# Performance work log

Hardware: AMD Instinct MI355X
Metric: run time of the kernel (lower is better)

## Reference

```python
import jax, jax.numpy as jnp
import numpy as np

B, S, D = 4, 4096, 1024

def setup_inputs() -> dict:
    key = jax.random.key(0)
    k1, k2, k3 = jax.random.split(key, 3)
    x = jax.random.normal(k1, (B, S, D), dtype=jnp.float32)
    # torch nn.Linear weights: [out_features, in_features], scaled for sanity
    W_qkv = jax.random.normal(k2, (3 * D, D), dtype=jnp.float32) * (1.0 / np.sqrt(D))
    W_o = jax.random.normal(k3, (D, D), dtype=jnp.float32) * (1.0 / np.sqrt(D))
    return {"x": x, "W_qkv": W_qkv, "W_o": W_o}


def reference(x, W_qkv, W_o):
    d_model = x.shape[-1]
    # torch Linear: y = x @ W.T
    qkv = jnp.einsum("bsd,ed->bse", x, W_qkv)  # [B, S, 3D]
    Q, K, V = jnp.split(qkv, 3, axis=-1)
    scale = 1.0 / jnp.sqrt(jnp.asarray(d_model, dtype=x.dtype))
    logits = jnp.einsum("bqd,bkd->bqk", Q, K) * scale  # [B, S, S]
    weights = jax.nn.softmax(logits, axis=-1)
    attn = jnp.einsum("bqk,bkd->bqd", weights, V)  # [B, S, D]
    out = jnp.einsum("bsd,ed->bse", attn, W_o)  # [B, S, D]
    return out
```

## Files before the change

kernel.cpp:

```cpp
#include <hip/hip_runtime.h>
#include <hip/hip_bf16.h>
#include <stdint.h>

typedef unsigned short u16;
typedef __bf16 bf16x8 __attribute__((ext_vector_type(8)));
typedef unsigned short u16x8 __attribute__((ext_vector_type(8)));
typedef float f32x4 __attribute__((ext_vector_type(4)));

__device__ __forceinline__ float bf2f(u16 h) {
  union { uint32_t u; float f; } x;
  x.u = ((uint32_t)h) << 16;
  return x.f;
}
__device__ __forceinline__ u16 f2bf(float f) {
  union { float f; uint32_t u; } x;
  x.f = f;
  uint32_t r = x.u + 0x7FFFu + ((x.u >> 16) & 1u);
  return (u16)(r >> 16);
}

__device__ __forceinline__ void gload_lds16(const u16* g, u16* l) {
  __builtin_amdgcn_global_load_lds(
      (const __attribute__((address_space(1))) uint32_t*)g,
      (__attribute__((address_space(3))) uint32_t*)l, 16, 0, 0);
}

__global__ __launch_bounds__(256) void cvt_all(
    const float* __restrict__ x, const float* __restrict__ w1,
    const float* __restrict__ w2, u16* __restrict__ xb,
    u16* __restrict__ w1b, u16* __restrict__ w2b, int n1, int n2, int n3) {
  int i = blockIdx.x * 256 + threadIdx.x;
  const float* src;
  u16* dst;
  int j = i;
  if (i < n1) { src = x; dst = xb; }
  else if (i < n1 + n2) { src = w1; dst = w1b; j = i - n1; }
  else if (i < n1 + n2 + n3) { src = w2; dst = w2b; j = i - n1 - n2; }
  else return;
  const float4* p = (const float4*)src + (size_t)j * 2;
  float4 a = p[0], b = p[1];
  u16x8 o;
  o[0] = f2bf(a.x); o[1] = f2bf(a.y); o[2] = f2bf(a.z); o[3] = f2bf(a.w);
  o[4] = f2bf(b.x); o[5] = f2bf(b.y); o[6] = f2bf(b.z); o[7] = f2bf(b.w);
  ((u16x8*)dst)[j] = o;
}

template <typename OT, int EPI>
__global__ __launch_bounds__(256) void gemm_bt(
    const u16* __restrict__ A, int lda, long zsA,
    const u16* __restrict__ B, int ldb, long zsB,
    OT* __restrict__ C, int ldc, long zsC,
    int K, float scale, const float* __restrict__ rs) {
  const int z = blockIdx.z;
  A += (long)z * zsA;
  B += (long)z * zsB;
  C += (long)z * zsC;
  if constexpr (EPI == 2) rs += (long)z * 4096;

  __shared__ __align__(16) u16 As[2 * 128 * 32];
  __shared__ __align__(16) u16 Bs[2 * 128 * 32];
  const int tid  = threadIdx.x;
  const int m0   = blockIdx.y * 128;
  const int n0   = blockIdx.x * 128;
  const int wave = tid >> 6;
  const int lane = tid & 63;
  const int wm   = (wave >> 1) * 64;
  const int wn   = (wave & 1) * 64;
  const int l15  = lane & 15;
  const int quad = lane >> 4;

  f32x4 acc[4][4];
#pragma unroll
  for (int i = 0; i < 4; ++i)
#pragma unroll
    for (int j = 0; j < 4; ++j) acc[i][j] = f32x4{0.f, 0.f, 0.f, 0.f};

  const u16* gA0 = A + (size_t)(m0 + (tid >> 2)) * lda + (tid & 3) * 8;
  const u16* gA1 = A + (size_t)(m0 + 64 + (tid >> 2)) * lda + (tid & 3) * 8;
  const u16* gB0 = B + (size_t)(n0 + (tid >> 2)) * ldb + (tid & 3) * 8;
  const u16* gB1 = B + (size_t)(n0 + 64 + (tid >> 2)) * ldb + (tid & 3) * 8;
  u16* lA0 = As + tid * 8;
  u16* lA1 = As + (256 + tid) * 8;
  u16* lB0 = Bs + tid * 8;
  u16* lB1 = Bs + (256 + tid) * 8;

  for (int k0 = 0; k0 < K; k0 += 64) {
    __syncthreads();
#pragma unroll
    for (int s = 0; s < 2; ++s) {
      gload_lds16(gA0 + k0 + s * 32, lA0 + s * 4096);
      gload_lds16(gA1 + k0 + s * 32, lA1 + s * 4096);
      gload_lds16(gB0 + k0 + s * 32, lB0 + s * 4096);
      gload_lds16(gB1 + k0 + s * 32, lB1 + s * 4096);
    }
    __syncthreads();

#pragma unroll
    for (int s = 0; s < 2; ++s) {
      u16x8 a[4], b[4];
#pragma unroll
      for (int i = 0; i < 4; ++i)
        a[i] = *(const u16x8*)(As + s * 4096 + (wm + i * 16 + l15) * 32 + quad * 8);
#pragma unroll
      for (int j = 0; j < 4; ++j)
        b[j] = *(const u16x8*)(Bs + s * 4096 + (wn + j * 16 + l15) * 32 + quad * 8);
#pragma unroll
      for (int i = 0; i < 4; ++i)
#pragma unroll
        for (int j = 0; j < 4; ++j)
          acc[i][j] = __builtin_amdgcn_mfma_f32_16x16x32_bf16(
              __builtin_bit_cast(bf16x8, a[i]), __builtin_bit_cast(bf16x8, b[j]),
              acc[i][j], 0, 0, 0);
    }
  }

#pragma unroll
  for (int i = 0; i < 4; ++i) {
#pragma unroll
    for (int r = 0; r < 4; ++r) {
      const int row = m0 + wm + i * 16 + quad * 4 + r;
      float mul = scale;
      if constexpr (EPI == 2) mul = scale / rs[row];
      const size_t ro = (size_t)row * ldc;
#pragma unroll
      for (int j = 0; j < 4; ++j) {
        float v = acc[i][j][r] * mul;
        if constexpr (EPI == 1) v = __expf(v);
        const int col = n0 + wn + j * 16 + l15;
        if constexpr (__is_same(OT, float))
          C[ro + col] = v;
        else
          C[ro + col] = f2bf(v);
      }
    }
  }
}

#define BAR() __builtin_amdgcn_s_barrier()
#define PRIO(n) __builtin_amdgcn_s_setprio(n)
#define WAITV(n) asm volatile("s_waitcnt vmcnt(" #n ")" ::: "memory")

#define STG(c, h, q, t)                                                         \
  gload_lds16(((h) < 2 ? gAs : gBs) +                                           \
                  (size_t)(((h) & 1) * 128 + (q) * 64) * ((h) < 2 ? lda : ldb) + \
                  (size_t)(t) * 64,                                             \
              lds + (c) * 32768 + ((h) < 2 ? 0 : 16384) +                       \
                  (((h) & 1) * 8 + (q) * 4) * 1024 + wsub * 512)

#define LDA_Q(c, qm)                                                            \
  {                                                                             \
    _Pragma("unroll") for (int ii = 0; ii < 4; ++ii) {                          \
      _Pragma("unroll") for (int kk = 0; kk < 2; ++kk)                          \
          a[(qm) * 4 + ii][kk] = *(const u16x8*)(lds + (c) * 32768 +            \
              ((wm8 + (qm) * 4 + ii) * 2 + kk) * 512 + rq);                     \
    }                                                                           \
  }

#define LDB_Q(c, qn)                                                            \
  {                                                                             \
    _Pragma("unroll") for (int jj = 0; jj < 2; ++jj) {                          \
      _Pragma("unroll") for (int kk = 0; kk < 2; ++kk)                          \
          b[(qn) * 2 + jj][kk] = *(const u16x8*)(lds + (c) * 32768 + 16384 +    \
              ((wn4 + (qn) * 2 + jj) * 2 + kk) * 512 + rq);                     \
    }                                                                           \
  }

#define MFMA_Q(qm, qn)                                                          \
  {                                                                             \
    PRIO(1);                                                                    \
    _Pragma("unroll") for (int kk = 0; kk < 2; ++kk) {                          \
      _Pragma("unroll") for (int ii = 0; ii < 4; ++ii) {                        \
        _Pragma("unroll") for (int jj = 0; jj < 2; ++jj)                        \
            acc[(qm) * 4 + ii][(qn) * 2 + jj] =                                 \
                __builtin_amdgcn_mfma_f32_16x16x32_bf16(                        \
                    __builtin_bit_cast(bf16x8, a[(qm) * 4 + ii][kk]),           \
                    __builtin_bit_cast(bf16x8, b[(qn) * 2 + jj][kk]),           \
                    acc[(qm) * 4 + ii][(qn) * 2 + jj], 0, 0, 0);                \
      }                                                                         \
    }                                                                           \
    PRIO(0);                                                                    \
  }

template <typename OT, int EPI>
__global__ __launch_bounds__(512, 2) void gemm256(
    const u16* __restrict__ A, int lda, long zsA,
    const u16* __restrict__ B, int ldb, long zsB,
    OT* __restrict__ C, int ldc, long zsC,
    int K, float scale, const float* __restrict__ rs) {
  __shared__ __align__(16) u16 lds[65536];
  const int z = blockIdx.z;
  A += (long)z * zsA;
  B += (long)z * zsB;
  C += (long)z * zsC;
  if constexpr (EPI == 2) rs += (long)z * 4096;

  const int tid  = threadIdx.x;
  const int lane = tid & 63;
  const int w    = tid >> 6;
  const int wm   = w >> 2;
  const int wn   = w & 3;
  const int wm8  = wm * 8;
  const int wn4  = wn * 4;
  const int l15  = lane & 15;
  const int quad = lane >> 4;
  const int m0   = blockIdx.y * 256;
  const int n0   = blockIdx.x * 256;

  const int srow = (w >> 1) * 16 + (lane >> 2);
  const int kcol = ((lane & 3) * 8) ^ ((lane & 32) ? 16 : 0);
  const int skb  = w & 1;
  const u16* gAs = A + (size_t)(m0 + srow) * lda + skb * 32 + kcol;
  const u16* gBs = B + (size_t)(n0 + srow) * ldb + skb * 32 + kcol;
  const int wsub = (w >> 1) * 2 + skb;

  const int rq = (l15 * 32 + quad * 8) ^ ((l15 & 8) << 1);

  f32x4 acc[8][4];
#pragma unroll
  for (int i = 0; i < 8; ++i)
#pragma unroll
    for (int j = 0; j < 4; ++j) acc[i][j] = f32x4{0.f, 0.f, 0.f, 0.f};
  u16x8 a[8][2], b[4][2];

  const int ni = K >> 7;

#pragma unroll
  for (int h = 0; h < 4; ++h) { STG(0, h, 0, 0); STG(0, h, 1, 0); }
  STG(1, 0, 0, 1); STG(1, 0, 1, 1);
  STG(1, 1, 0, 1); STG(1, 1, 1, 1);
  WAITV(4);
  BAR();

  for (int i = 0; i < ni; ++i) {
    const int t1 = 2 * i + 1, t2 = 2 * i + 2, t3 = 2 * i + 3;
    const bool more = (i + 1 < ni);

    LDA_Q(0, 0); LDB_Q(0, 0);
    STG(1, 2, 0, t1); STG(1, 2, 1, t1);
    BAR(); MFMA_Q(0, 0); BAR();
    LDA_Q(0, 1); LDB_Q(0, 1);
    STG(1, 3, 0, t1); STG(1, 3, 1, t1);
    BAR(); MFMA_Q(0, 1); BAR();
    if (more) { STG(0, 0, 0, t2); STG(0, 0, 1, t2); }
    BAR(); MFMA_Q(1, 0); BAR();
    if (more) { STG(0, 1, 0, t2); STG(0, 1, 1, t2); WAITV(4); }
    else { WAITV(0); }
    BAR(); MFMA_Q(1, 1); BAR();
    LDA_Q(1, 0); LDB_Q(1, 0);
    if (more) { STG(0, 2, 0, t2); STG(0, 2, 1, t2); }
    BAR(); MFMA_Q(0, 0); BAR();
    LDA_Q(1, 1); LDB_Q(1, 1);
    if (more) { STG(0, 3, 0, t2); STG(0, 3, 1, t2); }
    BAR(); MFMA_Q(0, 1); BAR();
    if (more) { STG(1, 0, 0, t3); STG(1, 0, 1, t3); }
    BAR(); MFMA_Q(1, 0); BAR();
    if (more) { STG(1, 1, 0, t3); STG(1, 1, 1, t3); WAITV(4); }
    BAR(); MFMA_Q(1, 1); BAR();
  }

#pragma unroll
  for (int i = 0; i < 8; ++i) {
#pragma unroll
    for (int r = 0; r < 4; ++r) {
      const int row = m0 + wm * 128 + i * 16 + quad * 4 + r;
      float mul = scale;
      if constexpr (EPI == 2) mul = scale / rs[row];
      const size_t ro = (size_t)row * ldc;
#pragma unroll
      for (int j = 0; j < 4; ++j) {
        float v = acc[i][j][r] * mul;
        if constexpr (EPI == 1) v = __expf(v);
        const int col = n0 + wn * 64 + j * 16 + l15;
        if constexpr (__is_same(OT, float))
          C[ro + col] = v;
        else
          C[ro + col] = f2bf(v);
      }
    }
  }
}

__global__ __launch_bounds__(256) void rowsum_rows(
    const u16* __restrict__ P, long zsP, float* __restrict__ rs) {
  const int row = blockIdx.x;
  const int z   = blockIdx.y;
  const u16* p = P + (long)z * zsP + (size_t)row * 4096;
  const int tid  = threadIdx.x;
  const int lane = tid & 63;
  const int wave = tid >> 6;

  u16x8 h0 = *(const u16x8*)(p + tid * 16);
  u16x8 h1 = *(const u16x8*)(p + tid * 16 + 8);
  float s = 0.f;
#pragma unroll
  for (int j = 0; j < 8; ++j) s += bf2f(h0[j]) + bf2f(h1[j]);
  for (int o = 32; o > 0; o >>= 1) s += __shfl_xor(s, o, 64);
  __shared__ float red[4];
  if (lane == 0) red[wave] = s;
  __syncthreads();
  if (tid == 0) rs[(size_t)z * 4096 + row] = red[0] + red[1] + red[2] + red[3];
}

__global__ __launch_bounds__(256) void transpose_v(
    const u16* __restrict__ V, int ldv, long zsV,
    u16* __restrict__ Vt, int ldt, long zsT) {
  const int z = blockIdx.z;
  V  += (long)z * zsV;
  Vt += (long)z * zsT;
  __shared__ u16 T[64][65];
  const int d0 = blockIdx.x * 64;
  const int s0 = blockIdx.y * 64;
  const int tid = threadIdx.x;
  const int c = tid & 63;
  const int rbase = (tid >> 6) * 16;
#pragma unroll
  for (int r = 0; r < 16; ++r)
    T[rbase + r][c] = V[(size_t)(s0 + rbase + r) * ldv + d0 + c];
  __syncthreads();
#pragma unroll
  for (int r = 0; r < 16; ++r)
    Vt[(size_t)(d0 + rbase + r) * ldt + s0 + c] = T[c][rbase + r];
}

extern "C" void kernel_launch(void* const* d_in, const int* in_sizes, int n_in,
                              void* d_out, int out_size, void* d_ws, size_t ws_size,
                              hipStream_t stream) {
  const float* x    = (const float*)d_in[0];
  const float* Wqkv = (const float*)d_in[1];
  const float* Wo   = (const float*)d_in[2];
  float* out = (float*)d_out;

  const int Bn = 4, S = 4096, D = 1024;
  const int M = Bn * S;
  const int E = 3 * D;
  const long SE = (long)S * E, SS = (long)S * S, DS = (long)D * S, SD = (long)S * D;

  const int nz = (ws_size >= (size_t)226492416) ? 2 : 1;

  char* ws = (char*)d_ws;
  size_t off = 0;
  u16* qkv = (u16*)(ws + off);  off += (size_t)M * E * 2;
  u16* Sb  = (u16*)(ws + off);  off += (size_t)nz * S * S * 2;
  u16* Vt  = (u16*)(ws + off);  off += (size_t)nz * D * S * 2;
  u16* xb  = (u16*)(ws + off);  off += (size_t)M * D * 2;
  u16* attn = xb;
  u16* Wqkvb = (u16*)(ws + off); off += (size_t)E * D * 2;
  u16* Wob   = (u16*)(ws + off); off += (size_t)D * D * 2;
  float* rs = (float*)Wqkvb;

  const int n1 = M * D / 8, n2 = E * D / 8, n3 = D * D / 8;
  cvt_all<<<(n1 + n2 + n3 + 255) / 256, 256, 0, stream>>>(
      x, Wqkv, Wo, xb, Wqkvb, Wob, n1, n2, n3);

  gemm256<u16, 0><<<dim3(E / 256, M / 256, 1), 512, 0, stream>>>(
      xb, D, 0, Wqkvb, D, 0, qkv, E, 0, D, 1.0f, nullptr);

  const float scl = 0.03125f;
  for (int c = 0; c < Bn; c += nz) {
    const u16* Qc = qkv + (size_t)c * SE;
    transpose_v<<<dim3(D / 64, S / 64, nz), 256, 0, stream>>>(
        Qc + 2 * D, E, SE, Vt, S, DS);
    gemm256<u16, 1><<<dim3(S / 256, S / 256, nz), 512, 0, stream>>>(
        Qc, E, SE, Qc + D, E, SE, Sb, S, SS, D, scl, nullptr);
    rowsum_rows<<<dim3(S, nz), 256, 0, stream>>>(Sb, SS, rs);
    gemm_bt<u16, 2><<<dim3(D / 128, S / 128, nz), 256, 0, stream>>>(
        Sb, S, SS, Vt, S, DS, attn + (size_t)c * SD, D, SD, S, 1.0f, rs);
  }

  gemm256<float, 0><<<dim3(D / 256, M / 256, 1), 512, 0, stream>>>(
      attn, D, 0, Wob, D, 0, out, D, 0, D, 1.0f, nullptr);
}
```

Baseline: 665.6 us.

## Rework GEMM main loop with inline-asm LDS reads and restructured prefetch schedule

Replaces the compiler-generated LDS fragment loads with inline ds_read_b128 using immediate offsets, and restructures each phase as load fragments, issue global-to-LDS prefetches, barrier, wait lgkmcnt, then run the MFMAs behind sched_barriers. The double-buffer schedule changes: the prologue loads only one stage and waits fully, and each half-iteration prefetches the other buffer and ends with a full vmcnt(0) wait instead of partial waits. This is meant to cut address arithmetic and give explicit control over the instruction schedule. The full vmcnt waits and the reduced prefetch depth risk exposing global-load latency.

```diff
diff --git a/kernel.cpp b/kernel.cpp
--- a/kernel.cpp
+++ b/kernel.cpp
@@ -23,6 +23,14 @@
   __builtin_amdgcn_global_load_lds(
       (const __attribute__((address_space(1))) uint32_t*)g,
       (__attribute__((address_space(3))) uint32_t*)l, 16, 0, 0);
+}
+
+typedef __attribute__((address_space(3))) const u16 lds_cu16;
+template <int OFF>
+__device__ __forceinline__ f32x4 ds_read128o(const lds_cu16* p) {
+  f32x4 r;
+  asm volatile("ds_read_b128 %0, %1 offset:%2" : "=v"(r) : "v"(p), "n"(OFF));
+  return r;
 }
 
 __global__ __launch_bounds__(256) void cvt_all(
@@ -138,7 +146,12 @@
 
 #define BAR() __builtin_amdgcn_s_barrier()
 #define PRIO(n) __builtin_amdgcn_s_setprio(n)
-#define WAITV(n) asm volatile("s_waitcnt vmcnt(" #n ")" ::: "memory")
+#define WAITV(n) asm volatile("s_waitcnt vmcnt(" #n ")")
+#define WAITLGKM() asm volatile("s_waitcnt lgkmcnt(0)")
+#define SCHEDB() __builtin_amdgcn_sched_barrier(0)
+#define DSR(p, off) ds_read128o<(off)>(p)
+#define AO(qm, ii, kk) ((((qm) * 4 + (ii)) * 2 + (kk)) * 1024)
+#define BO(qn, jj, kk) ((((qn) * 2 + (jj)) * 2 + (kk)) * 1024)
 
 #define STG(c, h, q, t)                                                         \
   gload_lds16(((h) < 2 ? gAs : gBs) +                                           \
@@ -147,38 +160,37 @@
               lds + (c) * 32768 + ((h) < 2 ? 0 : 16384) +                       \
                   (((h) & 1) * 8 + (q) * 4) * 1024 + wsub * 512)
 
-#define LDA_Q(c, qm)                                                            \
+#define MM(qm, ii, qn, jj, AV, BV)                                              \
+  acc[(qm) * 4 + (ii)][(qn) * 2 + (jj)] =                                       \
+      __builtin_amdgcn_mfma_f32_16x16x32_bf16(                                  \
+          __builtin_bit_cast(bf16x8, AV), __builtin_bit_cast(bf16x8, BV),       \
+          acc[(qm) * 4 + (ii)][(qn) * 2 + (jj)], 0, 0, 0);
+
+#define PH(LA, LB, qm, qn, STGS, TAILW)                                         \
   {                                                                             \
-    _Pragma("unroll") for (int ii = 0; ii < 4; ++ii) {                          \
-      _Pragma("unroll") for (int kk = 0; kk < 2; ++kk)                          \
-          a[(qm) * 4 + ii][kk] = *(const u16x8*)(lds + (c) * 32768 +            \
-              ((wm8 + (qm) * 4 + ii) * 2 + kk) * 512 + rq);                     \
-    }                                                                           \
-  }
-
-#define LDB_Q(c, qn)                                                            \
-  {                                                                             \
-    _Pragma("unroll") for (int jj = 0; jj < 2; ++jj) {                          \
-      _Pragma("unroll") for (int kk = 0; kk < 2; ++kk)                          \
-          b[(qn) * 2 + jj][kk] = *(const u16x8*)(lds + (c) * 32768 + 16384 +    \
-              ((wn4 + (qn) * 2 + jj) * 2 + kk) * 512 + rq);                     \
-    }                                                                           \
-  }
-
-#define MFMA_Q(qm, qn)                                                          \
-  {                                                                             \
+    f32x4 a0k0 = DSR(LA, AO(qm, 0, 0)), a0k1 = DSR(LA, AO(qm, 0, 1));           \
+    f32x4 a1k0 = DSR(LA, AO(qm, 1, 0)), a1k1 = DSR(LA, AO(qm, 1, 1));           \
+    f32x4 a2k0 = DSR(LA, AO(qm, 2, 0)), a2k1 = DSR(LA, AO(qm, 2, 1));           \
+    f32x4 a3k0 = DSR(LA, AO(qm, 3, 0)), a3k1 = DSR(LA, AO(qm, 3, 1));           \
+    f32x4 b0k0 = DSR(LB, BO(qn, 0, 0)), b0k1 = DSR(LB, BO(qn, 0, 1));           \
+    f32x4 b1k0 = DSR(LB, BO(qn, 1, 0)), b1k1 = DSR(LB, BO(qn, 1, 1));           \
+    STGS                                                                        \
+    BAR();                                                                      \
+    WAITLGKM();                                                                 \
+    SCHEDB();                                                                   \
     PRIO(1);                                                                    \
-    _Pragma("unroll") for (int kk = 0; kk < 2; ++kk) {                          \
-      _Pragma("unroll") for (int ii = 0; ii < 4; ++ii) {                        \
-        _Pragma("unroll") for (int jj = 0; jj < 2; ++jj)                        \
-            acc[(qm) * 4 + ii][(qn) * 2 + jj] =                                 \
-                __builtin_amdgcn_mfma_f32_16x16x32_bf16(                        \
-                    __builtin_bit_cast(bf16x8, a[(qm) * 4 + ii][kk]),           \
-                    __builtin_bit_cast(bf16x8, b[(qn) * 2 + jj][kk]),           \
-                    acc[(qm) * 4 + ii][(qn) * 2 + jj], 0, 0, 0);                \
-      }                                                                         \
-    }                                                                           \
+    MM(qm, 0, qn, 0, a0k0, b0k0) MM(qm, 0, qn, 1, a0k0, b1k0)                   \
+    MM(qm, 1, qn, 0, a1k0, b0k0) MM(qm, 1, qn, 1, a1k0, b1k0)                   \
+    MM(qm, 2, qn, 0, a2k0, b0k0) MM(qm, 2, qn, 1, a2k0, b1k0)                   \
+    MM(qm, 3, qn, 0, a3k0, b0k0) MM(qm, 3, qn, 1, a3k0, b1k0)                   \
+    MM(qm, 0, qn, 0, a0k1, b0k1) MM(qm, 0, qn, 1, a0k1, b1k1)                   \
+    MM(qm, 1, qn, 0, a1k1, b0k1) MM(qm, 1, qn, 1, a1k1, b1k1)                   \
+    MM(qm, 2, qn, 0, a2k1, b0k1) MM(qm, 2, qn, 1, a2k1, b1k1)                   \
+    MM(qm, 3, qn, 0, a3k1, b0k1) MM(qm, 3, qn, 1, a3k1, b1k1)                   \
     PRIO(0);                                                                    \
+    SCHEDB();                                                                   \
+    TAILW                                                                       \
+    BAR();                                                                      \
   }
 
 template <typename OT, int EPI>
@@ -214,48 +226,43 @@
   const int wsub = (w >> 1) * 2 + skb;
 
   const int rq = (l15 * 32 + quad * 8) ^ ((l15 & 8) << 1);
+  const lds_cu16* Lp  = (const lds_cu16*)lds;
+  const lds_cu16* LA0 = Lp + wm8 * 1024 + rq;
+  const lds_cu16* LA1 = LA0 + 32768;
+  const lds_cu16* LB0 = Lp + 16384 + wn4 * 1024 + rq;
+  const lds_cu16* LB1 = LB0 + 32768;
 
   f32x4 acc[8][4];
 #pragma unroll
   for (int i = 0; i < 8; ++i)
 #pragma unroll
     for (int j = 0; j < 4; ++j) acc[i][j] = f32x4{0.f, 0.f, 0.f, 0.f};
-  u16x8 a[8][2], b[4][2];
 
   const int ni = K >> 7;
 
 #pragma unroll
   for (int h = 0; h < 4; ++h) { STG(0, h, 0, 0); STG(0, h, 1, 0); }
-  STG(1, 0, 0, 1); STG(1, 0, 1, 1);
-  STG(1, 1, 0, 1); STG(1, 1, 1, 1);
-  WAITV(4);
+  WAITV(0);
   BAR();
 
   for (int i = 0; i < ni; ++i) {
-    const int t1 = 2 * i + 1, t2 = 2 * i + 2, t3 = 2 * i + 3;
+    const int t1 = 2 * i + 1, t2 = 2 * i + 2;
     const bool more = (i + 1 < ni);
 
-    LDA_Q(0, 0); LDB_Q(0, 0);
-    STG(1, 2, 0, t1); STG(1, 2, 1, t1);
-    BAR(); MFMA_Q(0, 0); BAR();
-    LDA_Q(0, 1); LDB_Q(0, 1);
-    STG(1, 3, 0, t1); STG(1, 3, 1, t1);
-    BAR(); MFMA_Q(0, 1); BAR();
-    if (more) { STG(0, 0, 0, t2); STG(0, 0, 1, t2); }
-    BAR(); MFMA_Q(1, 0); BAR();
-    if (more) { STG(0, 1, 0, t2); STG(0, 1, 1, t2); WAITV(4); }
-    else { WAITV(0); }
-    BAR(); MFMA_Q(1, 1); BAR();
-    LDA_Q(1, 0); LDB_Q(1, 0);
-    if (more) { STG(0, 2, 0, t2); STG(0, 2, 1, t2); }
-    BAR(); MFMA_Q(0, 0); BAR();
-    LDA_Q(1, 1); LDB_Q(1, 1);
-    if (more) { STG(0, 3, 0, t2); STG(0, 3, 1, t2); }
-    BAR(); MFMA_Q(0, 1); BAR();
-    if (more) { STG(1, 0, 0, t3); STG(1, 0, 1, t3); }
-    BAR(); MFMA_Q(1, 0); BAR();
-    if (more) { STG(1, 1, 0, t3); STG(1, 1, 1, t3); WAITV(4); }
-    BAR(); MFMA_Q(1, 1); BAR();
+    PH(LA0, LB0, 0, 0,
+       STG(1, 0, 0, t1); STG(1, 0, 1, t1); STG(1, 1, 0, t1); STG(1, 1, 1, t1);, )
+    PH(LA0, LB0, 0, 1,
+       STG(1, 2, 0, t1); STG(1, 2, 1, t1); STG(1, 3, 0, t1); STG(1, 3, 1, t1);, )
+    PH(LA0, LB0, 1, 0, , )
+    PH(LA0, LB0, 1, 1, , WAITV(0);)
+    PH(LA1, LB1, 0, 0,
+       if (more) { STG(0, 0, 0, t2); STG(0, 0, 1, t2);
+                   STG(0, 1, 0, t2); STG(0, 1, 1, t2); }, )
+    PH(LA1, LB1, 0, 1,
+       if (more) { STG(0, 2, 0, t2); STG(0, 2, 1, t2);
+                   STG(0, 3, 0, t2); STG(0, 3, 1, t2); }, )
+    PH(LA1, LB1, 1, 0, , )
+    PH(LA1, LB1, 1, 1, , WAITV(0);)
   }
 
 #pragma unroll
```

New measurement: 629.8 us. 1.06x faster.
